# Performance work log

Measured on AMD Instinct MI355X. Metric: run time of the kernel, lower is better.

The kernel has to match this reference:

```python
import jax, jax.numpy as jnp
import numpy as np

B, T, D = 4, 2048, 1024
N_HEADS = 16
HEAD_DIM = D // N_HEADS


def setup_inputs() -> dict:
    key = jax.random.key(0)
    ks = jax.random.split(key, 12)
    s = 1.0 / np.sqrt(D)
    return {
        "query": jax.random.normal(ks[0], (B, T, D), jnp.float32),
        "key_value": jax.random.normal(ks[1], (B, T, D), jnp.float32),
        "Wq": jax.random.uniform(ks[2], (D, D), jnp.float32, -s, s),
        "bq": jax.random.uniform(ks[3], (D,), jnp.float32, -s, s),
        "Wk": jax.random.uniform(ks[4], (D, D), jnp.float32, -s, s),
        "bk": jax.random.uniform(ks[5], (D,), jnp.float32, -s, s),
        "Wv": jax.random.uniform(ks[6], (D, D), jnp.float32, -s, s),
        "bv": jax.random.uniform(ks[7], (D,), jnp.float32, -s, s),
        "Wo": jax.random.uniform(ks[8], (D, D), jnp.float32, -s, s),
        "bo": jax.random.uniform(ks[9], (D,), jnp.float32, -s, s),
        "lookahead": 128,
    }


def reference(query, key_value, Wq, bq, Wk, bk, Wv, bv, Wo, bo, lookahead):
    b, t, d = query.shape
    scale = HEAD_DIM ** -0.5
    # projections: [B,T,D] -> [B,H,T,hd]
    def split_heads(x):
        return x.reshape(b, t, N_HEADS, HEAD_DIM).transpose(0, 2, 1, 3)
    Q = split_heads(query @ Wq.T + bq)
    K = split_heads(key_value @ Wk.T + bk)
    V = split_heads(key_value @ Wv.T + bv)
    # banded causal mask: key j allowed iff j <= i + lookahead
    i = jnp.arange(t)[:, None]
    j = jnp.arange(t)[None, :]
    allowed = j <= i + lookahead  # [T,T] bool
    scores = jnp.einsum('bhqd,bhkd->bhqk', Q, K) * scale
    scores = jnp.where(allowed, scores, -jnp.inf)
    attn = jax.nn.softmax(scores, axis=-1)  # dropout p=0.0 (eval)
    out = jnp.einsum('bhqk,bhkd->bhqd', attn, V)
    out = out.transpose(0, 2, 1, 3).reshape(b, t, d)
    return out @ Wo.T + bo
```

## Files before the change

kernel.cpp:

```cpp
#include <hip/hip_runtime.h>
#include <hip/hip_bf16.h>

typedef __attribute__((ext_vector_type(8))) short short8;
typedef __attribute__((ext_vector_type(4))) float f32x4;
typedef __attribute__((ext_vector_type(16))) float f32x16;

#define LOG2E 1.44269504088896340736f

__global__ __launch_bounds__(256) void k_cvtX(const float* __restrict__ q_in,
                                              const float* __restrict__ kv_in,
                                              __hip_bfloat16* __restrict__ Xq) {
  int i = blockIdx.x * blockDim.x + threadIdx.x;
  const int stride = gridDim.x * blockDim.x;
  for (; i < 4194304; i += stride) {
    const float4 v = (i < 2097152) ? reinterpret_cast<const float4*>(q_in)[i]
                                   : reinterpret_cast<const float4*>(kv_in)[i - 2097152];
    union { __hip_bfloat16 h[4]; short4 s; } p;
    p.h[0] = __float2bfloat16(v.x);
    p.h[1] = __float2bfloat16(v.y);
    p.h[2] = __float2bfloat16(v.z);
    p.h[3] = __float2bfloat16(v.w);
    reinterpret_cast<short4*>(Xq)[i] = p.s;
  }
}

__global__ __launch_bounds__(256) void k_cvtW(const float* __restrict__ Wq,
                                              const float* __restrict__ Wk,
                                              const float* __restrict__ Wv,
                                              const float* __restrict__ Wo,
                                              __hip_bfloat16* __restrict__ Wqkv,
                                              __hip_bfloat16* __restrict__ Wob) {
  int i = blockIdx.x * blockDim.x + threadIdx.x;
  const int stride = gridDim.x * blockDim.x;
  for (; i < 1048576; i += stride) {
    float4 v;
    short4* dst;
    if (i < 786432) {
      const float4* src = (i < 262144) ? reinterpret_cast<const float4*>(Wq)
                         : (i < 524288) ? reinterpret_cast<const float4*>(Wk)
                                        : reinterpret_cast<const float4*>(Wv);
      v = src[i & 262143];
      dst = reinterpret_cast<short4*>(Wqkv) + i;
    } else {
      v = reinterpret_cast<const float4*>(Wo)[i - 786432];
      dst = reinterpret_cast<short4*>(Wob) + (i - 786432);
    }
    union { __hip_bfloat16 h[4]; short4 s; } p;
    p.h[0] = __float2bfloat16(v.x);
    p.h[1] = __float2bfloat16(v.y);
    p.h[2] = __float2bfloat16(v.z);
    p.h[3] = __float2bfloat16(v.w);
    *dst = p.s;
  }
}

__device__ __forceinline__ void gload_lds16(const __hip_bfloat16* g, __hip_bfloat16* l) {
  __builtin_amdgcn_global_load_lds(
      (const __attribute__((address_space(1))) unsigned int*)g,
      (__attribute__((address_space(3))) unsigned int*)l, 16, 0, 0);
}

__device__ __forceinline__ unsigned pk_bf16(float a, float b) {
  union { __hip_bfloat16 h; unsigned short u; } x, y;
  x.h = __float2bfloat16(a);
  y.h = __float2bfloat16(b);
  return (unsigned)x.u | ((unsigned)y.u << 16);
}

__device__ __forceinline__ void plswap2(unsigned a, unsigned b, unsigned& x, unsigned& y) {
#if __has_builtin(__builtin_amdgcn_permlane32_swap)
  auto r = __builtin_amdgcn_permlane32_swap(a, b, false, false);
  x = r[0];
  y = r[1];
#else
  unsigned d, s;
  asm volatile("v_mov_b32 %0, %2\n\tv_mov_b32 %1, %3\n\tv_permlane32_swap_b32 %0, %1"
               : "=&v"(d), "=&v"(s)
               : "v"(a), "v"(b));
  x = d;
  y = s;
#endif
}

template <int NB, int OUTMODE>
__global__ __launch_bounds__(256, 4) void k_gemm(
    const __hip_bfloat16* __restrict__ Aq, const __hip_bfloat16* __restrict__ Akv,
    const __hip_bfloat16* __restrict__ Wt,
    const float* __restrict__ b0p, const float* __restrict__ b1p, const float* __restrict__ b2p,
    __hip_bfloat16* __restrict__ Obf, float* __restrict__ Of) {
  const int K = 1024;
  __shared__ __hip_bfloat16 As[3][4096];
  __shared__ __hip_bfloat16 Bs[3][4096];
  const int tid = threadIdx.x;
  const int lane = tid & 63;
  const int w = tid >> 6;
  const int wr = w >> 1, wc = w & 1;
  const int lg = lane >> 4, lr = lane & 15;

  const int bid = blockIdx.x;
  const int xcd = bid & 7, idx = bid >> 3;
  const int m0 = (xcd * 8 + idx / NB) * 128;
  const int n0 = (idx % NB) * 128;

  const int proj = (OUTMODE == 0) ? (n0 >> 10) : 0;
  const __hip_bfloat16* A = (OUTMODE == 0) ? (proj == 0 ? Aq : Akv) : Aq;

  const f32x4 fzero = {0.f, 0.f, 0.f, 0.f};
  f32x4 acc[4][4];
#pragma unroll
  for (int i = 0; i < 4; i++)
#pragma unroll
    for (int j = 0; j < 4; j++) acc[i][j] = fzero;

  const int c0 = w * 2;
  const int srow = lane >> 2;
  const int scol = (lane & 3) * 8;

  auto STAGE = [&](int kt, int buf) {
    const int k0 = kt * 32;
#pragma unroll
    for (int i = 0; i < 2; i++) {
      const int c = c0 + i;
      const int row = c * 16 + srow;
      gload_lds16(A + (size_t)(m0 + row) * K + k0 + scol, As[buf] + c * 512);
      gload_lds16(Wt + (size_t)(n0 + row) * K + k0 + scol, Bs[buf] + c * 512);
    }
  };

  STAGE(0, 0);

  int cur = 0;
  for (int kt = 0; kt < 32; ++kt) {
    if (kt + 1 < 32) {
      const int nb = (cur == 2) ? 0 : cur + 1;
      STAGE(kt + 1, nb);
      asm volatile("s_waitcnt vmcnt(4)" ::: "memory");
    } else {
      asm volatile("s_waitcnt vmcnt(0)" ::: "memory");
    }
    __builtin_amdgcn_s_barrier();

    const int bc = cur;
    short8 af[4], bfr[4];
#pragma unroll
    for (int mi = 0; mi < 4; mi++)
      af[mi] = *(const short8*)(As[bc] + (wr * 64 + mi * 16 + lr) * 32 + lg * 8);
#pragma unroll
    for (int ni = 0; ni < 4; ni++)
      bfr[ni] = *(const short8*)(Bs[bc] + (wc * 64 + ni * 16 + lr) * 32 + lg * 8);
#pragma unroll
    for (int mi = 0; mi < 4; mi++)
#pragma unroll
      for (int ni = 0; ni < 4; ni++)
        acc[mi][ni] = __builtin_amdgcn_mfma_f32_16x16x32_bf16(af[mi], bfr[ni], acc[mi][ni], 0, 0, 0);
    cur = (cur == 2) ? 0 : cur + 1;
  }

  const float scale = (OUTMODE == 0 && proj == 0) ? (0.125f * LOG2E) : 1.0f;
  const float* bias = (OUTMODE == 0) ? (proj == 0 ? b0p : (proj == 1 ? b1p : b2p)) : b0p;
  __hip_bfloat16* Ob = (OUTMODE == 0) ? (Obf + (size_t)proj * 8388608) : nullptr;

#pragma unroll
  for (int mi = 0; mi < 4; mi++) {
#pragma unroll
    for (int ni = 0; ni < 4; ni++) {
      const int n = n0 + wc * 64 + ni * 16 + lr;
      const float bn = bias[n & 1023];
#pragma unroll
      for (int r = 0; r < 4; r++) {
        const int m = m0 + wr * 64 + mi * 16 + lg * 4 + r;
        const float v = (acc[mi][ni][r] + bn) * scale;
        if (OUTMODE == 0) {
          const int b = m >> 11, t = m & 2047;
          const int h = (n >> 6) & 15, d = n & 63;
          Ob[(((size_t)(b * 16 + h)) * 2048 + t) * 64 + d] = __float2bfloat16(v);
        } else {
          Of[(size_t)m * 1024 + n] = v;
        }
      }
    }
  }
}

__global__ __launch_bounds__(256) void k_transpose(const __hip_bfloat16* __restrict__ V,
                                                   __hip_bfloat16* __restrict__ Vt) {
  __shared__ __hip_bfloat16 tile[64][72];
  const int bh = blockIdx.y;
  const int t0 = blockIdx.x * 64;
  const int tid = threadIdx.x;
#pragma unroll
  for (int it = 0; it < 2; ++it) {
    const int r = it * 32 + (tid >> 3);
    const int c = (tid & 7) * 8;
    short8 v = *(const short8*)(V + ((size_t)bh * 2048 + t0 + r) * 64 + c);
    *(short8*)(&tile[r][c]) = v;
  }
  __syncthreads();
#pragma unroll
  for (int it = 0; it < 2; ++it) {
    const int d = it * 32 + (tid >> 3);
    const int tt = (tid & 7) * 8;
    __hip_bfloat16 tmp[8];
#pragma unroll
    for (int j = 0; j < 8; j++) tmp[j] = tile[tt + j][d];
    *(short8*)(Vt + ((size_t)bh * 64 + d) * 2048 + t0 + tt) = *(short8*)tmp;
  }
}

__global__ __launch_bounds__(512, 2) void k_attn6(const __hip_bfloat16* __restrict__ Qm,
                                                  const __hip_bfloat16* __restrict__ Km,
                                                  const __hip_bfloat16* __restrict__ Vt,
                                                  __hip_bfloat16* __restrict__ O,
                                                  const int* __restrict__ la_ptr) {
  const int T = 2048;
  __shared__ __hip_bfloat16 Ks[3][4096];
  __shared__ __hip_bfloat16 Vs[3][4096];
  const int tid = threadIdx.x;
  const int lane = tid & 63;
  const int w = tid >> 6;
  const int hi = lane >> 5;
  const int l31 = lane & 31;

  const int l = blockIdx.y * 8 + blockIdx.x;
  const int half = l >> 8;
  const int u = l & 255;
  const int xi = u & 7;
  const int yi = u >> 3;
  const int qblk = half ? xi : (7 - xi);
  const int bh = yi + (half << 5);

  const int q0 = qblk * 256;
  const int la = *la_ptr;
  const int qw = q0 + w * 32;
  const int q = qw + l31;

  short8 qf[4];
  {
    const __hip_bfloat16* qrow = Qm + ((size_t)bh * T + q) * 64;
#pragma unroll
    for (int ks = 0; ks < 4; ks++) qf[ks] = *(const short8*)(qrow + ks * 16 + hi * 8);
  }

  f32x16 acc0, acc1;
#pragma unroll
  for (int r = 0; r < 16; r++) { acc0[r] = 0.f; acc1[r] = 0.f; }
  float lsum = 0.f;

  const int kend_w = min(T, qw + 32 + la);
  const int kend_b = min(T, q0 + 256 + la);
  const int ntiles = (kend_b + 63) >> 6;

  const int srow = tid >> 3;
  const int sc16 = (tid & 7) ^ (srow & 7);
  const __hip_bfloat16* Kg = Km + (size_t)bh * T * 64 + (size_t)srow * 64 + sc16 * 8;
  const __hip_bfloat16* Vg = Vt + (size_t)bh * 64 * T + (size_t)srow * T + sc16 * 8;
  const int kswz = l31 & 7;

  auto STAGEKV = [&](int t, int buf) {
    gload_lds16(Kg + (size_t)(t << 6) * 64, Ks[buf] + w * 512);
    gload_lds16(Vg + (t << 6), Vs[buf] + w * 512);
  };

  auto QK = [&](const __hip_bfloat16* Ksc, int kt2) {
    const int krow = kt2 * 32 + l31;
    f32x16 s;
#pragma unroll
    for (int r = 0; r < 16; r++) s[r] = 0.f;
    __builtin_amdgcn_s_setprio(1);
#pragma unroll
    for (int ks = 0; ks < 4; ks++) {
      short8 kf = *(const short8*)((const char*)Ksc + krow * 128 +
                                   ((((ks << 1) | hi)) ^ kswz) * 16);
      s = __builtin_amdgcn_mfma_f32_32x32x16_bf16(kf, qf[ks], s, 0, 0, 0);
    }
    __builtin_amdgcn_s_setprio(0);
    return s;
  };

  auto SMPV = [&](f32x16& s, int kb32, int kt2, const __hip_bfloat16* Vsc) {
    if (kb32 + 31 > qw + la) {
      const int thr = q + la - kb32;
#pragma unroll
      for (int r = 0; r < 16; r++) {
        const int crow = (r & 3) + ((r >> 2) << 3) + (hi << 2);
        if (crow > thr) s[r] = -1e30f;
      }
    }
    float e[16];
#pragma unroll
    for (int i = 0; i < 16; i++) e[i] = exp2f(s[i]);
    float p01 = (e[0] + e[1]) + (e[2] + e[3]);
    float p23 = (e[4] + e[5]) + (e[6] + e[7]);
    float p45 = (e[8] + e[9]) + (e[10] + e[11]);
    float p67 = (e[12] + e[13]) + (e[14] + e[15]);
    lsum += (p01 + p23) + (p45 + p67);
    unsigned W[8];
#pragma unroll
    for (int i = 0; i < 8; i++) W[i] = pk_bf16(e[2 * i], e[2 * i + 1]);

    int4 A0, A1;
    {
      unsigned x0, z0, y0, w0, x1, z1, y1, w1;
      plswap2(W[0], W[2], x0, z0);
      plswap2(W[1], W[3], y0, w0);
      plswap2(W[4], W[6], x1, z1);
      plswap2(W[5], W[7], y1, w1);
      A0.x = (int)x0; A0.y = (int)y0; A0.z = (int)z0; A0.w = (int)w0;
      A1.x = (int)x1; A1.y = (int)y1; A1.z = (int)z1; A1.w = (int)w1;
    }

    __builtin_amdgcn_s_setprio(1);
#pragma unroll
    for (int ks2 = 0; ks2 < 2; ks2++) {
      union { int4 i; short8 s8; } pa;
      pa.i = ks2 ? A1 : A0;
      const int ksg = kt2 * 2 + ks2;
      const int col16 = ((ksg << 1) | hi);
      short8 vf0 = *(const short8*)((const char*)Vsc + l31 * 128 + ((col16 ^ kswz)) * 16);
      short8 vf1 = *(const short8*)((const char*)Vsc + (32 + l31) * 128 + ((col16 ^ kswz)) * 16);
      acc0 = __builtin_amdgcn_mfma_f32_32x32x16_bf16(vf0, pa.s8, acc0, 0, 0, 0);
      acc1 = __builtin_amdgcn_mfma_f32_32x32x16_bf16(vf1, pa.s8, acc1, 0, 0, 0);
    }
    __builtin_amdgcn_s_setprio(0);
  };

  STAGEKV(0, 0);

  int cur = 0, nxt = 1;
  for (int kt = 0; kt < ntiles; ++kt) {
    const int kbase = kt << 6;
    if (kt + 1 < ntiles) {
      STAGEKV(kt + 1, nxt);
      asm volatile("s_waitcnt vmcnt(2)" ::: "memory");
    } else {
      asm volatile("s_waitcnt vmcnt(0)" ::: "memory");
    }
    __builtin_amdgcn_s_barrier();

    if (kbase < kend_w) {
      const __hip_bfloat16* Ksc = Ks[cur];
      const __hip_bfloat16* Vsc = Vs[cur];
      const bool d1 = (kbase + 32) < kend_w;
      f32x16 sA = QK(Ksc, 0);
      f32x16 sB;
      if (d1) sB = QK(Ksc, 1);
      SMPV(sA, kbase, 0, Vsc);
      if (d1) SMPV(sB, kbase + 32, 1, Vsc);
    }
    cur = nxt;
    nxt = (nxt == 2) ? 0 : nxt + 1;
  }

  {
    unsigned r0, r1;
    plswap2(__float_as_uint(lsum), __float_as_uint(lsum), r0, r1);
    lsum = __uint_as_float(r0) + __uint_as_float(r1);
  }
  const float rinv = 1.f / lsum;
  const int b = bh >> 4, h = bh & 15;
  __hip_bfloat16* orow = O + ((size_t)(b * T + q)) * 1024 + h * 64;
#pragma unroll
  for (int rq = 0; rq < 4; rq++) {
    const int d0 = rq * 8 + hi * 4;
    union { __hip_bfloat16 h4[4]; short4 s4; } o;
#pragma unroll
    for (int j = 0; j < 4; j++) o.h4[j] = __float2bfloat16(acc0[rq * 4 + j] * rinv);
    *(short4*)(orow + d0) = o.s4;
  }
#pragma unroll
  for (int rq = 0; rq < 4; rq++) {
    const int d0 = rq * 8 + hi * 4 + 32;
    union { __hip_bfloat16 h4[4]; short4 s4; } o;
#pragma unroll
    for (int j = 0; j < 4; j++) o.h4[j] = __float2bfloat16(acc1[rq * 4 + j] * rinv);
    *(short4*)(orow + d0) = o.s4;
  }
}

extern "C" void kernel_launch(void* const* d_in, const int* in_sizes, int n_in,
                              void* d_out, int out_size, void* d_ws, size_t ws_size,
                              hipStream_t stream) {
  const float* q_in = (const float*)d_in[0];
  const float* kv_in = (const float*)d_in[1];
  const float* Wq = (const float*)d_in[2];
  const float* bq = (const float*)d_in[3];
  const float* Wk = (const float*)d_in[4];
  const float* bk = (const float*)d_in[5];
  const float* Wv = (const float*)d_in[6];
  const float* bv = (const float*)d_in[7];
  const float* Wo = (const float*)d_in[8];
  const float* bo = (const float*)d_in[9];
  const int* la = (const int*)d_in[10];

  char* ws = (char*)d_ws;
  const size_t SZX = (size_t)8192 * 1024 * 2;
  const size_t SZW = (size_t)1024 * 1024 * 2;
  __hip_bfloat16* Xq = (__hip_bfloat16*)(ws);
  __hip_bfloat16* Xkv = (__hip_bfloat16*)(ws + SZX);
  __hip_bfloat16* Wqkv = (__hip_bfloat16*)(ws + 2 * SZX);
  __hip_bfloat16* Wob = (__hip_bfloat16*)(ws + 2 * SZX + 3 * SZW);
  __hip_bfloat16* Qb = (__hip_bfloat16*)(ws + 2 * SZX + 4 * SZW);
  __hip_bfloat16* Kb = (__hip_bfloat16*)(ws + 3 * SZX + 4 * SZW);
  __hip_bfloat16* Vb = (__hip_bfloat16*)(ws + 4 * SZX + 4 * SZW);
  __hip_bfloat16* Vtb = (__hip_bfloat16*)(ws);
  __hip_bfloat16* AOb = (__hip_bfloat16*)(ws + SZX);

  k_cvtX<<<4096, 256, 0, stream>>>(q_in, kv_in, Xq);
  k_cvtW<<<2048, 256, 0, stream>>>(Wq, Wk, Wv, Wo, Wqkv, Wob);

  k_gemm<24, 0><<<1536, 256, 0, stream>>>(Xq, Xkv, Wqkv, bq, bk, bv, Qb, nullptr);
  k_transpose<<<dim3(32, 64), 256, 0, stream>>>(Vb, Vtb);
  k_attn6<<<dim3(8, 64), 512, 0, stream>>>(Qb, Kb, Vtb, AOb, la);
  k_gemm<8, 1><<<512, 256, 0, stream>>>(AOb, AOb, Wob, bo, bo, bo, nullptr, (float*)d_out);

  (void)Kb;
}
```

Baseline: 217.2 us.

## Fuse V transpose into QKV GEMM epilogue and software-pipeline attention PV

The QKV projection GEMM now writes the V projection directly in transposed [bh, d, t] layout, which removes the separate transpose kernel and its extra global round trip. The attention kernel moves to 4-deep K/V shared buffers and defers the second half-tile's PV MFMA into the next iteration, so it overlaps with the next QK computation. The transposed writes from the GEMM epilogue are strided along t and may coalesce poorly. The larger LDS footprint could also reduce occupancy.

```diff
diff --git a/kernel.cpp b/kernel.cpp
--- a/kernel.cpp
+++ b/kernel.cpp
@@ -87,7 +87,8 @@
     const __hip_bfloat16* __restrict__ Aq, const __hip_bfloat16* __restrict__ Akv,
     const __hip_bfloat16* __restrict__ Wt,
     const float* __restrict__ b0p, const float* __restrict__ b1p, const float* __restrict__ b2p,
-    __hip_bfloat16* __restrict__ Obf, float* __restrict__ Of) {
+    __hip_bfloat16* __restrict__ Obf, __hip_bfloat16* __restrict__ Vtb,
+    float* __restrict__ Of) {
   const int K = 1024;
   __shared__ __hip_bfloat16 As[3][4096];
   __shared__ __hip_bfloat16 Bs[3][4096];
@@ -173,7 +174,11 @@
         if (OUTMODE == 0) {
           const int b = m >> 11, t = m & 2047;
           const int h = (n >> 6) & 15, d = n & 63;
-          Ob[(((size_t)(b * 16 + h)) * 2048 + t) * 64 + d] = __float2bfloat16(v);
+          if (proj == 2) {
+            Vtb[(((size_t)(b * 16 + h)) * 64 + d) * 2048 + t] = __float2bfloat16(v);
+          } else {
+            Ob[(((size_t)(b * 16 + h)) * 2048 + t) * 64 + d] = __float2bfloat16(v);
+          }
         } else {
           Of[(size_t)m * 1024 + n] = v;
         }
@@ -182,39 +187,14 @@
   }
 }
 
-__global__ __launch_bounds__(256) void k_transpose(const __hip_bfloat16* __restrict__ V,
-                                                   __hip_bfloat16* __restrict__ Vt) {
-  __shared__ __hip_bfloat16 tile[64][72];
-  const int bh = blockIdx.y;
-  const int t0 = blockIdx.x * 64;
-  const int tid = threadIdx.x;
-#pragma unroll
-  for (int it = 0; it < 2; ++it) {
-    const int r = it * 32 + (tid >> 3);
-    const int c = (tid & 7) * 8;
-    short8 v = *(const short8*)(V + ((size_t)bh * 2048 + t0 + r) * 64 + c);
-    *(short8*)(&tile[r][c]) = v;
-  }
-  __syncthreads();
-#pragma unroll
-  for (int it = 0; it < 2; ++it) {
-    const int d = it * 32 + (tid >> 3);
-    const int tt = (tid & 7) * 8;
-    __hip_bfloat16 tmp[8];
-#pragma unroll
-    for (int j = 0; j < 8; j++) tmp[j] = tile[tt + j][d];
-    *(short8*)(Vt + ((size_t)bh * 64 + d) * 2048 + t0 + tt) = *(short8*)tmp;
-  }
-}
-
-__global__ __launch_bounds__(512, 2) void k_attn6(const __hip_bfloat16* __restrict__ Qm,
+__global__ __launch_bounds__(512, 2) void k_attn7(const __hip_bfloat16* __restrict__ Qm,
                                                   const __hip_bfloat16* __restrict__ Km,
                                                   const __hip_bfloat16* __restrict__ Vt,
                                                   __hip_bfloat16* __restrict__ O,
                                                   const int* __restrict__ la_ptr) {
   const int T = 2048;
-  __shared__ __hip_bfloat16 Ks[3][4096];
-  __shared__ __hip_bfloat16 Vs[3][4096];
+  __shared__ __hip_bfloat16 Ks[4][4096];
+  __shared__ __hip_bfloat16 Vs[4][4096];
   const int tid = threadIdx.x;
   const int lane = tid & 63;
   const int w = tid >> 6;
@@ -326,30 +306,37 @@
 
   STAGEKV(0, 0);
 
-  int cur = 0, nxt = 1;
+  f32x16 sB;
+  bool haveB = false;
+  int pendKb = 0;
   for (int kt = 0; kt < ntiles; ++kt) {
     const int kbase = kt << 6;
     if (kt + 1 < ntiles) {
-      STAGEKV(kt + 1, nxt);
+      STAGEKV(kt + 1, (kt + 1) & 3);
       asm volatile("s_waitcnt vmcnt(2)" ::: "memory");
     } else {
       asm volatile("s_waitcnt vmcnt(0)" ::: "memory");
     }
     __builtin_amdgcn_s_barrier();
 
-    if (kbase < kend_w) {
-      const __hip_bfloat16* Ksc = Ks[cur];
-      const __hip_bfloat16* Vsc = Vs[cur];
+    const bool act = kbase < kend_w;
+    f32x16 sA;
+    if (act) sA = QK(Ks[kt & 3], 0);
+    if (haveB) {
+      SMPV(sB, pendKb, 1, Vs[(kt - 1) & 3]);
+      haveB = false;
+    }
+    if (act) {
       const bool d1 = (kbase + 32) < kend_w;
-      f32x16 sA = QK(Ksc, 0);
-      f32x16 sB;
-      if (d1) sB = QK(Ksc, 1);
-      SMPV(sA, kbase, 0, Vsc);
-      if (d1) SMPV(sB, kbase + 32, 1, Vsc);
-    }
-    cur = nxt;
-    nxt = (nxt == 2) ? 0 : nxt + 1;
-  }
+      if (d1) sB = QK(Ks[kt & 3], 1);
+      SMPV(sA, kbase, 0, Vs[kt & 3]);
+      if (d1) {
+        haveB = true;
+        pendKb = kbase + 32;
+      }
+    }
+  }
+  if (haveB) SMPV(sB, pendKb, 1, Vs[(ntiles - 1) & 3]);
 
   {
     unsigned r0, r1;
@@ -401,17 +388,13 @@
   __hip_bfloat16* Wob = (__hip_bfloat16*)(ws + 2 * SZX + 3 * SZW);
   __hip_bfloat16* Qb = (__hip_bfloat16*)(ws + 2 * SZX + 4 * SZW);
   __hip_bfloat16* Kb = (__hip_bfloat16*)(ws + 3 * SZX + 4 * SZW);
-  __hip_bfloat16* Vb = (__hip_bfloat16*)(ws + 4 * SZX + 4 * SZW);
-  __hip_bfloat16* Vtb = (__hip_bfloat16*)(ws);
+  __hip_bfloat16* Vtb = (__hip_bfloat16*)(ws + 4 * SZX + 4 * SZW);
   __hip_bfloat16* AOb = (__hip_bfloat16*)(ws + SZX);
 
   k_cvtX<<<4096, 256, 0, stream>>>(q_in, kv_in, Xq);
   k_cvtW<<<2048, 256, 0, stream>>>(Wq, Wk, Wv, Wo, Wqkv, Wob);
 
-  k_gemm<24, 0><<<1536, 256, 0, stream>>>(Xq, Xkv, Wqkv, bq, bk, bv, Qb, nullptr);
-  k_transpose<<<dim3(32, 64), 256, 0, stream>>>(Vb, Vtb);
-  k_attn6<<<dim3(8, 64), 512, 0, stream>>>(Qb, Kb, Vtb, AOb, la);
-  k_gemm<8, 1><<<512, 256, 0, stream>>>(AOb, AOb, Wob, bo, bo, bo, nullptr, (float*)d_out);
-
-  (void)Kb;
-}
+  k_gemm<24, 0><<<1536, 256, 0, stream>>>(Xq, Xkv, Wqkv, bq, bk, bv, Qb, Vtb, nullptr);
+  k_attn7<<<dim3(8, 64), 512, 0, stream>>>(Qb, Kb, Vtb, AOb, la);
+  k_gemm<8, 1><<<512, 256, 0, stream>>>(AOb, AOb, Wob, bo, bo, bo, nullptr, nullptr, (float*)d_out);
+}
```

New measurement: 227.1 us. +4.6%, slower.

## Split attention key range across waves and reduce partial sums in LDS

Applied to the files above, without the earlier changes.

Rewrites the attention kernel so each 256-thread block handles one 32-query tile per head, with its four waves splitting the key tiles and combining partial accumulators and row sums through shared memory. K and V fragments are now read straight from global memory instead of going through a barrier-synchronised, triple-buffered LDS pipeline. V is stored as contiguous 64x64 blocks so each block's loads are local. This gives a much larger grid with finer load balance and no per-tile barriers. In exchange, K/V reuse across query tiles now depends on cache hits rather than explicit LDS sharing, and the final reduction adds LDS traffic.

```diff
diff --git a/kernel.cpp b/kernel.cpp
--- a/kernel.cpp
+++ b/kernel.cpp
@@ -182,11 +182,12 @@
   }
 }
 
-__global__ __launch_bounds__(256) void k_transpose(const __hip_bfloat16* __restrict__ V,
-                                                   __hip_bfloat16* __restrict__ Vt) {
+__global__ __launch_bounds__(256) void k_vblock(const __hip_bfloat16* __restrict__ V,
+                                                __hip_bfloat16* __restrict__ Vblk) {
   __shared__ __hip_bfloat16 tile[64][72];
   const int bh = blockIdx.y;
-  const int t0 = blockIdx.x * 64;
+  const int kt = blockIdx.x;
+  const int t0 = kt * 64;
   const int tid = threadIdx.x;
 #pragma unroll
   for (int it = 0; it < 2; ++it) {
@@ -196,6 +197,7 @@
     *(short8*)(&tile[r][c]) = v;
   }
   __syncthreads();
+  __hip_bfloat16* out = Vblk + ((size_t)(bh * 32 + kt)) * 4096;
 #pragma unroll
   for (int it = 0; it < 2; ++it) {
     const int d = it * 32 + (tid >> 3);
@@ -203,36 +205,34 @@
     __hip_bfloat16 tmp[8];
 #pragma unroll
     for (int j = 0; j < 8; j++) tmp[j] = tile[tt + j][d];
-    *(short8*)(Vt + ((size_t)bh * 64 + d) * 2048 + t0 + tt) = *(short8*)tmp;
-  }
-}
-
-__global__ __launch_bounds__(512, 2) void k_attn6(const __hip_bfloat16* __restrict__ Qm,
+    *(short8*)(out + d * 64 + tt) = *(short8*)tmp;
+  }
+}
+
+__global__ __launch_bounds__(256, 2) void k_attn9(const __hip_bfloat16* __restrict__ Qm,
                                                   const __hip_bfloat16* __restrict__ Km,
-                                                  const __hip_bfloat16* __restrict__ Vt,
+                                                  const __hip_bfloat16* __restrict__ Vblk,
                                                   __hip_bfloat16* __restrict__ O,
                                                   const int* __restrict__ la_ptr) {
   const int T = 2048;
-  __shared__ __hip_bfloat16 Ks[3][4096];
-  __shared__ __hip_bfloat16 Vs[3][4096];
+  __shared__ float accb[3][64][36];
+  __shared__ float lsb[3][64];
   const int tid = threadIdx.x;
   const int lane = tid & 63;
   const int w = tid >> 6;
   const int hi = lane >> 5;
   const int l31 = lane & 31;
 
-  const int l = blockIdx.y * 8 + blockIdx.x;
-  const int half = l >> 8;
-  const int u = l & 255;
-  const int xi = u & 7;
-  const int yi = u >> 3;
-  const int qblk = half ? xi : (7 - xi);
-  const int bh = yi + (half << 5);
-
-  const int q0 = qblk * 256;
+  const int bh = blockIdx.x;
+  const int qt = 63 - blockIdx.y;
   const int la = *la_ptr;
-  const int qw = q0 + w * 32;
+  const int qw = qt << 5;
   const int q = qw + l31;
+
+  const int kend = min(T, qw + 32 + la);
+  const int nkt = (kend + 63) >> 6;
+  const int t0 = (w * nkt) >> 2;
+  const int t1 = ((w + 1) * nkt) >> 2;
 
   short8 qf[4];
   {
@@ -241,114 +241,75 @@
     for (int ks = 0; ks < 4; ks++) qf[ks] = *(const short8*)(qrow + ks * 16 + hi * 8);
   }
 
-  f32x16 acc0, acc1;
-#pragma unroll
-  for (int r = 0; r < 16; r++) { acc0[r] = 0.f; acc1[r] = 0.f; }
+  f32x16 acc0, acc1, fz;
+#pragma unroll
+  for (int r = 0; r < 16; r++) { acc0[r] = 0.f; acc1[r] = 0.f; fz[r] = 0.f; }
   float lsum = 0.f;
 
-  const int kend_w = min(T, qw + 32 + la);
-  const int kend_b = min(T, q0 + 256 + la);
-  const int ntiles = (kend_b + 63) >> 6;
-
-  const int srow = tid >> 3;
-  const int sc16 = (tid & 7) ^ (srow & 7);
-  const __hip_bfloat16* Kg = Km + (size_t)bh * T * 64 + (size_t)srow * 64 + sc16 * 8;
-  const __hip_bfloat16* Vg = Vt + (size_t)bh * 64 * T + (size_t)srow * T + sc16 * 8;
-  const int kswz = l31 & 7;
-
-  auto STAGEKV = [&](int t, int buf) {
-    gload_lds16(Kg + (size_t)(t << 6) * 64, Ks[buf] + w * 512);
-    gload_lds16(Vg + (t << 6), Vs[buf] + w * 512);
-  };
-
-  auto QK = [&](const __hip_bfloat16* Ksc, int kt2) {
-    const int krow = kt2 * 32 + l31;
-    f32x16 s;
-#pragma unroll
-    for (int r = 0; r < 16; r++) s[r] = 0.f;
-    __builtin_amdgcn_s_setprio(1);
-#pragma unroll
-    for (int ks = 0; ks < 4; ks++) {
-      short8 kf = *(const short8*)((const char*)Ksc + krow * 128 +
-                                   ((((ks << 1) | hi)) ^ kswz) * 16);
-      s = __builtin_amdgcn_mfma_f32_32x32x16_bf16(kf, qf[ks], s, 0, 0, 0);
-    }
-    __builtin_amdgcn_s_setprio(0);
-    return s;
-  };
-
-  auto SMPV = [&](f32x16& s, int kb32, int kt2, const __hip_bfloat16* Vsc) {
-    if (kb32 + 31 > qw + la) {
-      const int thr = q + la - kb32;
-#pragma unroll
-      for (int r = 0; r < 16; r++) {
-        const int crow = (r & 3) + ((r >> 2) << 3) + (hi << 2);
-        if (crow > thr) s[r] = -1e30f;
-      }
-    }
-    float e[16];
-#pragma unroll
-    for (int i = 0; i < 16; i++) e[i] = exp2f(s[i]);
-    float p01 = (e[0] + e[1]) + (e[2] + e[3]);
-    float p23 = (e[4] + e[5]) + (e[6] + e[7]);
-    float p45 = (e[8] + e[9]) + (e[10] + e[11]);
-    float p67 = (e[12] + e[13]) + (e[14] + e[15]);
-    lsum += (p01 + p23) + (p45 + p67);
-    unsigned W[8];
-#pragma unroll
-    for (int i = 0; i < 8; i++) W[i] = pk_bf16(e[2 * i], e[2 * i + 1]);
-
-    int4 A0, A1;
-    {
-      unsigned x0, z0, y0, w0, x1, z1, y1, w1;
-      plswap2(W[0], W[2], x0, z0);
-      plswap2(W[1], W[3], y0, w0);
-      plswap2(W[4], W[6], x1, z1);
-      plswap2(W[5], W[7], y1, w1);
-      A0.x = (int)x0; A0.y = (int)y0; A0.z = (int)z0; A0.w = (int)w0;
-      A1.x = (int)x1; A1.y = (int)y1; A1.z = (int)z1; A1.w = (int)w1;
-    }
-
-    __builtin_amdgcn_s_setprio(1);
-#pragma unroll
-    for (int ks2 = 0; ks2 < 2; ks2++) {
-      union { int4 i; short8 s8; } pa;
-      pa.i = ks2 ? A1 : A0;
-      const int ksg = kt2 * 2 + ks2;
-      const int col16 = ((ksg << 1) | hi);
-      short8 vf0 = *(const short8*)((const char*)Vsc + l31 * 128 + ((col16 ^ kswz)) * 16);
-      short8 vf1 = *(const short8*)((const char*)Vsc + (32 + l31) * 128 + ((col16 ^ kswz)) * 16);
-      acc0 = __builtin_amdgcn_mfma_f32_32x32x16_bf16(vf0, pa.s8, acc0, 0, 0, 0);
-      acc1 = __builtin_amdgcn_mfma_f32_32x32x16_bf16(vf1, pa.s8, acc1, 0, 0, 0);
-    }
-    __builtin_amdgcn_s_setprio(0);
-  };
-
-  STAGEKV(0, 0);
-
-  int cur = 0, nxt = 1;
-  for (int kt = 0; kt < ntiles; ++kt) {
+  const __hip_bfloat16* Kg = Km + (size_t)bh * T * 64;
+  const __hip_bfloat16* Vg = Vblk + (size_t)bh * 32 * 4096;
+
+  for (int kt = t0; kt < t1; ++kt) {
     const int kbase = kt << 6;
-    if (kt + 1 < ntiles) {
-      STAGEKV(kt + 1, nxt);
-      asm volatile("s_waitcnt vmcnt(2)" ::: "memory");
-    } else {
-      asm volatile("s_waitcnt vmcnt(0)" ::: "memory");
-    }
-    __builtin_amdgcn_s_barrier();
-
-    if (kbase < kend_w) {
-      const __hip_bfloat16* Ksc = Ks[cur];
-      const __hip_bfloat16* Vsc = Vs[cur];
-      const bool d1 = (kbase + 32) < kend_w;
-      f32x16 sA = QK(Ksc, 0);
-      f32x16 sB;
-      if (d1) sB = QK(Ksc, 1);
-      SMPV(sA, kbase, 0, Vsc);
-      if (d1) SMPV(sB, kbase + 32, 1, Vsc);
-    }
-    cur = nxt;
-    nxt = (nxt == 2) ? 0 : nxt + 1;
+    const __hip_bfloat16* vb = Vg + (size_t)kt * 4096;
+#pragma unroll
+    for (int kt2 = 0; kt2 < 2; ++kt2) {
+      const int kb32 = kbase + kt2 * 32;
+      if (kb32 >= kend) break;
+
+      const __hip_bfloat16* kp = Kg + (size_t)(kb32 + l31) * 64 + hi * 8;
+      __builtin_amdgcn_s_setprio(1);
+      f32x16 s = __builtin_amdgcn_mfma_f32_32x32x16_bf16(*(const short8*)(kp), qf[0], fz, 0, 0, 0);
+      s = __builtin_amdgcn_mfma_f32_32x32x16_bf16(*(const short8*)(kp + 16), qf[1], s, 0, 0, 0);
+      s = __builtin_amdgcn_mfma_f32_32x32x16_bf16(*(const short8*)(kp + 32), qf[2], s, 0, 0, 0);
+      s = __builtin_amdgcn_mfma_f32_32x32x16_bf16(*(const short8*)(kp + 48), qf[3], s, 0, 0, 0);
+      __builtin_amdgcn_s_setprio(0);
+
+      if (kb32 + 31 > qw + la) {
+        const int thr = q + la - kb32;
+#pragma unroll
+        for (int r = 0; r < 16; r++) {
+          const int crow = (r & 3) + ((r >> 2) << 3) + (hi << 2);
+          if (crow > thr) s[r] = -1e30f;
+        }
+      }
+
+      float e[16];
+#pragma unroll
+      for (int i = 0; i < 16; i++) e[i] = exp2f(s[i]);
+      float p01 = (e[0] + e[1]) + (e[2] + e[3]);
+      float p23 = (e[4] + e[5]) + (e[6] + e[7]);
+      float p45 = (e[8] + e[9]) + (e[10] + e[11]);
+      float p67 = (e[12] + e[13]) + (e[14] + e[15]);
+      lsum += (p01 + p23) + (p45 + p67);
+      unsigned W[8];
+#pragma unroll
+      for (int i = 0; i < 8; i++) W[i] = pk_bf16(e[2 * i], e[2 * i + 1]);
+
+      int4 A0, A1;
+      {
+        unsigned x0, z0, y0, w0, x1, z1, y1, w1;
+        plswap2(W[0], W[2], x0, z0);
+        plswap2(W[1], W[3], y0, w0);
+        plswap2(W[4], W[6], x1, z1);
+        plswap2(W[5], W[7], y1, w1);
+        A0.x = (int)x0; A0.y = (int)y0; A0.z = (int)z0; A0.w = (int)w0;
+        A1.x = (int)x1; A1.y = (int)y1; A1.z = (int)z1; A1.w = (int)w1;
+      }
+
+      __builtin_amdgcn_s_setprio(1);
+#pragma unroll
+      for (int ks2 = 0; ks2 < 2; ks2++) {
+        union { int4 i; short8 s8; } pa;
+        pa.i = ks2 ? A1 : A0;
+        const int col16 = (((kt2 * 2 + ks2) << 1) | hi);
+        short8 vf0 = *(const short8*)(vb + l31 * 64 + col16 * 8);
+        short8 vf1 = *(const short8*)(vb + (32 + l31) * 64 + col16 * 8);
+        acc0 = __builtin_amdgcn_mfma_f32_32x32x16_bf16(vf0, pa.s8, acc0, 0, 0, 0);
+        acc1 = __builtin_amdgcn_mfma_f32_32x32x16_bf16(vf1, pa.s8, acc1, 0, 0, 0);
+      }
+      __builtin_amdgcn_s_setprio(0);
+    }
   }
 
   {
@@ -356,24 +317,45 @@
     plswap2(__float_as_uint(lsum), __float_as_uint(lsum), r0, r1);
     lsum = __uint_as_float(r0) + __uint_as_float(r1);
   }
-  const float rinv = 1.f / lsum;
-  const int b = bh >> 4, h = bh & 15;
-  __hip_bfloat16* orow = O + ((size_t)(b * T + q)) * 1024 + h * 64;
-#pragma unroll
-  for (int rq = 0; rq < 4; rq++) {
-    const int d0 = rq * 8 + hi * 4;
-    union { __hip_bfloat16 h4[4]; short4 s4; } o;
-#pragma unroll
-    for (int j = 0; j < 4; j++) o.h4[j] = __float2bfloat16(acc0[rq * 4 + j] * rinv);
-    *(short4*)(orow + d0) = o.s4;
-  }
-#pragma unroll
-  for (int rq = 0; rq < 4; rq++) {
-    const int d0 = rq * 8 + hi * 4 + 32;
-    union { __hip_bfloat16 h4[4]; short4 s4; } o;
-#pragma unroll
-    for (int j = 0; j < 4; j++) o.h4[j] = __float2bfloat16(acc1[rq * 4 + j] * rinv);
-    *(short4*)(orow + d0) = o.s4;
+
+  if (w > 0) {
+#pragma unroll
+    for (int r = 0; r < 16; r++) {
+      accb[w - 1][lane][r] = acc0[r];
+      accb[w - 1][lane][16 + r] = acc1[r];
+    }
+    lsb[w - 1][lane] = lsum;
+  }
+  __syncthreads();
+  if (w == 0) {
+#pragma unroll
+    for (int w2 = 0; w2 < 3; w2++) {
+#pragma unroll
+      for (int r = 0; r < 16; r++) {
+        acc0[r] += accb[w2][lane][r];
+        acc1[r] += accb[w2][lane][16 + r];
+      }
+      lsum += lsb[w2][lane];
+    }
+    const float rinv = 1.f / lsum;
+    const int b = bh >> 4, h = bh & 15;
+    __hip_bfloat16* orow = O + ((size_t)(b * T + q)) * 1024 + h * 64;
+#pragma unroll
+    for (int rq = 0; rq < 4; rq++) {
+      const int d0 = rq * 8 + hi * 4;
+      union { __hip_bfloat16 h4[4]; short4 s4; } o;
+#pragma unroll
+      for (int j = 0; j < 4; j++) o.h4[j] = __float2bfloat16(acc0[rq * 4 + j] * rinv);
+      *(short4*)(orow + d0) = o.s4;
+    }
+#pragma unroll
+    for (int rq = 0; rq < 4; rq++) {
+      const int d0 = rq * 8 + hi * 4 + 32;
+      union { __hip_bfloat16 h4[4]; short4 s4; } o;
+#pragma unroll
+      for (int j = 0; j < 4; j++) o.h4[j] = __float2bfloat16(acc1[rq * 4 + j] * rinv);
+      *(short4*)(orow + d0) = o.s4;
+    }
   }
 }
 
@@ -402,16 +384,16 @@
   __hip_bfloat16* Qb = (__hip_bfloat16*)(ws + 2 * SZX + 4 * SZW);
   __hip_bfloat16* Kb = (__hip_bfloat16*)(ws + 3 * SZX + 4 * SZW);
   __hip_bfloat16* Vb = (__hip_bfloat16*)(ws + 4 * SZX + 4 * SZW);
-  __hip_bfloat16* Vtb = (__hip_bfloat16*)(ws);
+  __hip_bfloat16* Vblk = (__hip_bfloat16*)(ws);
   __hip_bfloat16* AOb = (__hip_bfloat16*)(ws + SZX);
 
   k_cvtX<<<4096, 256, 0, stream>>>(q_in, kv_in, Xq);
   k_cvtW<<<2048, 256, 0, stream>>>(Wq, Wk, Wv, Wo, Wqkv, Wob);
 
   k_gemm<24, 0><<<1536, 256, 0, stream>>>(Xq, Xkv, Wqkv, bq, bk, bv, Qb, nullptr);
-  k_transpose<<<dim3(32, 64), 256, 0, stream>>>(Vb, Vtb);
-  k_attn6<<<dim3(8, 64), 512, 0, stream>>>(Qb, Kb, Vtb, AOb, la);
+  k_vblock<<<dim3(32, 64), 256, 0, stream>>>(Vb, Vblk);
+  k_attn9<<<dim3(64, 64), 256, 0, stream>>>(Qb, Kb, Vblk, AOb, la);
   k_gemm<8, 1><<<512, 256, 0, stream>>>(AOb, AOb, Wob, bo, bo, bo, nullptr, (float*)d_out);
 
-  (void)Kb;
-}
+  (void)Vb;
+}
```

Result: slower. 279.0 us (+28.5%).
